# Kernel optimization log

Measured on AMD Instinct MI355X. Metric: run time of the kernel, lower is better.

The kernel has to match this reference:

```python
import jax, jax.numpy as jnp
import numpy as np

DIM = 2048
HEAD_DIM = 128
H = DIM // HEAD_DIM          # num ttt heads = 16
D_H = 128                    # inter_multi = 1.0 -> d_h = head_dim
CHUNK = 2048                 # lact_chunk_size
B, L = 1, 8192
BASE_LR = 0.01
LN_EPS = 1e-6                # flax LayerNorm default
NS_COEFS = [(4.0848, -6.8946, 2.927), (3.9505, -6.3029, 2.6377),
            (3.7418, -5.5913, 2.3037), (2.8769, -3.1427, 1.2046),
            (2.8366, -3.0525, 1.2012)]


def silu(x):
    return x * jax.nn.sigmoid(x)


def silu_backprop(dy, x):
    s = jax.nn.sigmoid(x)
    return dy * s * (1 + x * (1 - s))


def l2_norm(x, eps=1e-5):
    return x / (jnp.linalg.norm(x, axis=-1, keepdims=True) + eps)


def zeropower_ns5(G):
    # 5-step Newton-Schulz orthogonalization on a batch of matrices (bh, m, n)
    X = G
    transposed = G.shape[1] > G.shape[2]
    if transposed:
        X = jnp.swapaxes(X, 1, 2)
    X = X / (jnp.linalg.norm(X, axis=(1, 2), keepdims=True) + 1e-7)
    for a, b, c in NS_COEFS:
        A = X @ jnp.swapaxes(X, 1, 2)
        Bm = b * A + c * (A @ A)
        X = a * X + Bm @ X
    if transposed:
        X = jnp.swapaxes(X, 1, 2)
    return X


def block_causal_lact_swiglu(w0, w1, w2, q, k, v, lr0, lr1, lr2, momentum):
    # w0,w2: (bh, d_h, d); w1: (bh, d, d_h); q,k,v: (bh, l, d); lr*: (bh, l, 1)
    bh, l, d = k.shape
    v = jnp.swapaxes(v, 1, 2)   # (bh, d, l)
    q = jnp.swapaxes(q, 1, 2)   # (bh, d, l)
    w0_norm = jnp.linalg.norm(w0, axis=2, keepdims=True)
    w1_norm = jnp.linalg.norm(w1, axis=2, keepdims=True)
    w2_norm = jnp.linalg.norm(w2, axis=2, keepdims=True)
    outs = []
    for i in range(0, l - CHUNK, CHUNK):
        s, e = i, i + CHUNK
        ki = k[:, s:e, :]                      # (bh, C, d)
        vi = v[:, :, s:e]                      # (bh, d, C)
        qi = q[:, :, s:e]                      # (bh, d, C)
        lr0i, lr1i, lr2i = lr0[:, s:e, :], lr1[:, s:e, :], lr2[:, s:e, :]
        # apply current fast weights to queries
        h = w2 @ qi                            # (bh, d_h, C)
        gate = silu(w0 @ qi)
        outs.append(w1 @ (gate * h))           # (bh, d, C)
        # manual SwiGLU backprop through keys to get fast-weight grads
        kiT = jnp.swapaxes(ki, 1, 2)           # (bh, d, C)
        gate_before = w0 @ kiT                 # (bh, d_h, C)
        hidden_before = w2 @ kiT               # (bh, d_h, C)
        hidden = silu(gate_before) * hidden_before
        dhidden = jnp.swapaxes(w1, 1, 2) @ vi  # (bh, d_h, C)
        dhidden_before = dhidden * silu(gate_before)
        dgate = dhidden * hidden_before
        dgate_before = silu_backprop(dgate, gate_before)
        lr1iT = jnp.swapaxes(lr1i, 1, 2)       # (bh, 1, C) per-token lr
        dw1 = vi @ jnp.swapaxes(hidden * lr1iT, 1, 2)   # (bh, d, d_h)
        dw0 = dgate_before @ (ki * lr0i)                # (bh, d_h, d)
        dw2 = dhidden_before @ (ki * lr2i)              # (bh, d_h, d)
        if momentum is not None:
            m_i = jnp.mean(momentum[:, s:e, :], axis=1, keepdims=True)  # (bh,1,1)
            dw0 = dw0 + dw0 * m_i
            dw1 = dw1 + dw1 * m_i
            dw2 = dw2 + dw2 * m_i
        dw0 = zeropower_ns5(dw0)
        dw1 = zeropower_ns5(dw1)
        dw2 = zeropower_ns5(dw2)
        w0 = w0 + dw0
        w1 = w1 + dw1
        w2 = w2 + dw2
        # renormalize rows back to the initial norms
        w0 = w0 / (jnp.linalg.norm(w0, axis=2, keepdims=True) + 1e-5) * w0_norm
        w1 = w1 / (jnp.linalg.norm(w1, axis=2, keepdims=True) + 1e-5) * w1_norm
        w2 = w2 / (jnp.linalg.norm(w2, axis=2, keepdims=True) + 1e-5) * w2_norm
    # final chunk: apply only
    qi = q[:, :, l - CHUNK:]
    h = w2 @ qi
    gate = silu(w0 @ qi)
    outs.append(w1 @ (gate * h))
    out = jnp.concatenate(outs, axis=2)        # (bh, d, l)
    return jnp.swapaxes(out, 1, 2)             # (bh, l, d)


def _forward(x, W_qkv, W_lr, W_o, W_m, b_m, W_s, b_s, ln_g, ln_b, w0, w1, w2):
    b, l, _ = x.shape
    h, d = H, HEAD_DIM
    qkv = silu(x @ W_qkv).reshape(b, l, h, 3 * d)
    ttt_q, ttt_k, ttt_v = jnp.split(qkv, 3, axis=-1)
    ttt_q = l2_norm(ttt_q).reshape(b * h, l, d)
    ttt_k = l2_norm(ttt_k).reshape(b * h, l, d)
    ttt_v = ttt_v.reshape(b * h, l, d)
    base_lr_inv = BASE_LR + jnp.log(-jnp.expm1(jnp.float32(-BASE_LR)))
    lr = jax.nn.softplus(x @ W_lr + base_lr_inv)                 # (b, l, 3h)
    lr = lr.reshape(b, l, 3, h).transpose(2, 0, 3, 1).reshape(3, b * h, l, 1)
    lr0, lr1, lr2 = lr[0], lr[1], lr[2]
    w0b = jnp.tile(w0, (b, 1, 1))
    w1b = jnp.tile(w1, (b, 1, 1))
    w2b = jnp.tile(w2, (b, 1, 1))
    momentum = jax.nn.sigmoid(x @ W_m + b_m)                     # (b, l, h)
    momentum = momentum.reshape(b, l, h, 1).transpose(0, 2, 1, 3).reshape(b * h, l, 1)
    out = block_causal_lact_swiglu(w0b, w1b, w2b, ttt_q, ttt_k, ttt_v,
                                   lr0, lr1, lr2, momentum)      # (bh, l, d)
    # LayerNorm over last dim (flax default eps)
    mu = jnp.mean(out, axis=-1, keepdims=True)
    var = jnp.mean(jnp.square(out - mu), axis=-1, keepdims=True)
    out = (out - mu) * jax.lax.rsqrt(var + LN_EPS) * ln_g + ln_b
    scale = silu(x @ W_s + b_s).reshape(b, l, h, 1).transpose(0, 2, 1, 3).reshape(b * h, l, 1)
    out = out * scale
    out = out.reshape(b, h, l, d).transpose(0, 2, 1, 3).reshape(b, l, h * d)
    return out @ W_o


def setup_inputs() -> dict:
    ks = jax.random.split(jax.random.key(0), 11)
    sd = 1.0 / np.sqrt(DIM)
    return {
        "x": jax.random.normal(ks[0], (B, L, DIM), jnp.float32),
        "W_qkv": jax.random.normal(ks[1], (DIM, 3 * DIM), jnp.float32) * sd,
        "W_lr": jax.random.normal(ks[2], (DIM, 3 * H), jnp.float32) * sd,
        "W_o": jax.random.normal(ks[3], (DIM, DIM), jnp.float32) * sd,
        "W_m": jax.random.normal(ks[4], (DIM, H), jnp.float32) * sd,
        "b_m": jnp.zeros((H,), jnp.float32),
        "W_s": jax.random.normal(ks[5], (DIM, H), jnp.float32) * sd,
        "b_s": jnp.zeros((H,), jnp.float32),
        "ln_g": jnp.ones((HEAD_DIM,), jnp.float32),
        "ln_b": jnp.zeros((HEAD_DIM,), jnp.float32),
        "w0": jax.random.normal(ks[6], (H, D_H, HEAD_DIM), jnp.float32) / np.sqrt(HEAD_DIM),
        "w1": jax.random.normal(ks[7], (H, HEAD_DIM, D_H), jnp.float32) / np.sqrt(D_H),
        "w2": jax.random.normal(ks[8], (H, D_H, HEAD_DIM), jnp.float32) / np.sqrt(HEAD_DIM),
    }


def reference(x, W_qkv, W_lr, W_o, W_m, b_m, W_s, b_s, ln_g, ln_b, w0, w1, w2):
    return _forward(x, W_qkv, W_lr, W_o, W_m, b_m, W_s, b_s, ln_g, ln_b, w0, w1, w2)
```

## Files before the change

kernel.cpp:

```cpp
#include <hip/hip_runtime.h>
#include <hip/hip_bf16.h>
#include <cstdint>
#include <cstddef>

#define LSEQ   8192
#define DMODEL 2048
#define NH     16
#define HD     128
#define CH     2048

typedef __attribute__((ext_vector_type(8))) __bf16 bf16x8;
typedef __attribute__((ext_vector_type(4))) float f32x4;


__device__ __forceinline__ float wave_sum64(float v) {
#pragma unroll
  for (int m = 32; m; m >>= 1) v += __shfl_xor(v, m, 64);
  return v;
}

__device__ __forceinline__ float sigm(float x) { return 1.0f / (1.0f + expf(-x)); }

__device__ __forceinline__ unsigned short f2bf(float f) {
  unsigned int u = __float_as_uint(f);
  u += 0x7FFFu + ((u >> 16) & 1u);
  return (unsigned short)(u >> 16);
}
__device__ __forceinline__ float bf2f(unsigned short h) {
  return __uint_as_float((unsigned int)h << 16);
}

__device__ __forceinline__ void gload_lds16(const void* g, void* l) {
  __builtin_amdgcn_global_load_lds((__attribute__((address_space(1))) void*)(g),
                                   (__attribute__((address_space(3))) void*)(l), 16, 0, 0);
}

union bfu8 { bf16x8 v; unsigned short u[8]; };


__global__ void k_cast(const float* __restrict__ X, unsigned short* __restrict__ Xb, int n4) {
  int i = blockIdx.x * 256 + threadIdx.x;
  int stride = gridDim.x * 256;
  for (; i < n4; i += stride) {
    float4 v = ((const float4*)X)[i];
    ushort4 o;
    o.x = f2bf(v.x); o.y = f2bf(v.y); o.z = f2bf(v.z); o.w = f2bf(v.w);
    ((ushort4*)Xb)[i] = o;
  }
}

__global__ void k_tcast(const float* __restrict__ W, unsigned short* __restrict__ Wt,
                        int K, int N) {
  __shared__ float t[64][65];
  const int n0 = blockIdx.x * 64, k0 = blockIdx.y * 64;
  const int tid = threadIdx.x;
  const int cx = tid & 63, ry = tid >> 6;
#pragma unroll
  for (int r = 0; r < 16; ++r) {
    int row = ry + r * 4;
    t[row][cx] = W[(size_t)(k0 + row) * N + n0 + cx];
  }
  __syncthreads();
#pragma unroll
  for (int r = 0; r < 16; ++r) {
    int nn = ry + r * 4;
    Wt[(size_t)(n0 + nn) * K + k0 + cx] = f2bf(t[cx][nn]);
  }
}


__device__ __forceinline__ void gemm_core(const unsigned short* __restrict__ A,
                                          const unsigned short* __restrict__ B,
                                          int K, int ldA, int ldB, int row0, int col0,
                                          unsigned short* Al, unsigned short* Bl,
                                          f32x4 acc[4][4]) {
  const int tid = threadIdx.x;
  const int w = tid >> 6, l = tid & 63;
  const int lrow = l & 15, lk = (l >> 4) * 8;
  const int wr = (w >> 1) * 64, wc = (w & 1) * 64;
  const int srow = l >> 2, skk = (l & 3) * 8;

  for (int kk = 0; kk < K; kk += 32) {
#pragma unroll
    for (int q = 0; q < 2; ++q) {
      int c = w * 2 + q;
      gload_lds16(A + (size_t)(row0 + c * 16 + srow) * ldA + kk + skk, &Al[c * 512]);
      gload_lds16(B + (size_t)(col0 + c * 16 + srow) * ldB + kk + skk, &Bl[c * 512]);
    }
    __syncthreads();
    bf16x8 af[4], bfr[4];
#pragma unroll
    for (int m = 0; m < 4; ++m)
      af[m] = *(const bf16x8*)&Al[(wr + m * 16 + lrow) * 32 + lk];
#pragma unroll
    for (int n = 0; n < 4; ++n)
      bfr[n] = *(const bf16x8*)&Bl[(wc + n * 16 + lrow) * 32 + lk];
#pragma unroll
    for (int m = 0; m < 4; ++m)
#pragma unroll
      for (int n = 0; n < 4; ++n)
        acc[m][n] = __builtin_amdgcn_mfma_f32_16x16x32_bf16(af[m], bfr[n], acc[m][n], 0, 0, 0);
    __syncthreads();
  }
}


__device__ __forceinline__ bf16x8 ld_sw(const unsigned short* base, int row, int kcol) {
  int byte = (row * 256 + kcol * 2) ^ ((row & 7) << 4);
  return *(const bf16x8*)((const char*)base + byte);
}
__device__ __forceinline__ void st_sw(unsigned short* base, int row, int col, unsigned short v) {
  int byte = (row * 256 + col * 2) ^ ((row & 7) << 4);
  *(unsigned short*)((char*)base + byte) = v;
}
__device__ __forceinline__ unsigned short ld_sw1(const unsigned short* base, int row, int col) {
  int byte = (row * 256 + col * 2) ^ ((row & 7) << 4);
  return *(const unsigned short*)((const char*)base + byte);
}

__device__ __forceinline__ void stage_sw(const float* __restrict__ src, int ld,
                                         unsigned short* dst, int tid) {
#pragma unroll
  for (int p = 0; p < 16; ++p) {
    int row = p * 8 + (tid >> 5);
    int col = (tid & 31) * 4;
    float4 v = *(const float4*)(src + (size_t)row * ld + col);
    int byte = (row * 256 + col * 2) ^ ((row & 7) << 4);
    unsigned short* d = (unsigned short*)((char*)dst + byte);
    d[0] = f2bf(v.x); d[1] = f2bf(v.y); d[2] = f2bf(v.z); d[3] = f2bf(v.w);
  }
}

__device__ __forceinline__ void stage_hl(const float* __restrict__ src, int ld,
                                         unsigned short* H, unsigned short* L, int tid) {
#pragma unroll
  for (int p = 0; p < 16; ++p) {
    int row = p * 8 + (tid >> 5);
    int col = (tid & 31) * 4;
    float4 v = *(const float4*)(src + (size_t)row * ld + col);
    int byte = (row * 256 + col * 2) ^ ((row & 7) << 4);
    unsigned short* h = (unsigned short*)((char*)H + byte);
    unsigned short* l = (unsigned short*)((char*)L + byte);
    const float* pv = (const float*)&v;
#pragma unroll
    for (int i = 0; i < 4; ++i) {
      unsigned short hi = f2bf(pv[i]);
      h[i] = hi;
      l[i] = f2bf(pv[i] - bf2f(hi));
    }
  }
}

__device__ __forceinline__ void stage_hl_1024(const float* __restrict__ src, int ld,
                                              unsigned short* H, unsigned short* L, int tid) {
#pragma unroll
  for (int p = 0; p < 4; ++p) {
    int row = p * 32 + (tid >> 5);
    int col = (tid & 31) * 4;
    float4 v = *(const float4*)(src + (size_t)row * ld + col);
    int byte = (row * 256 + col * 2) ^ ((row & 7) << 4);
    unsigned short* h = (unsigned short*)((char*)H + byte);
    unsigned short* l = (unsigned short*)((char*)L + byte);
    const float* pv = (const float*)&v;
#pragma unroll
    for (int i = 0; i < 4; ++i) {
      unsigned short hi = f2bf(pv[i]);
      h[i] = hi;
      l[i] = f2bf(pv[i] - bf2f(hi));
    }
  }
}

__device__ __forceinline__ void stage_hl_ts(const float* __restrict__ src, int ld,
                                            const float* __restrict__ lr,
                                            unsigned short* H, unsigned short* L, int tid) {
#pragma unroll
  for (int p = 0; p < 16; ++p) {
    int t = p * 8 + (tid >> 5);
    int d = (tid & 31) * 4;
    float4 v = *(const float4*)(src + (size_t)t * ld + d);
    float sc = lr[t];
    const float* pv = (const float*)&v;
#pragma unroll
    for (int i = 0; i < 4; ++i) {
      float x = pv[i] * sc;
      unsigned short hi = f2bf(x);
      st_sw(H, d + i, t, hi);
      st_sw(L, d + i, t, f2bf(x - bf2f(hi)));
    }
  }
}


__global__ void k_init_w(const float* __restrict__ w0, const float* __restrict__ w1,
                         const float* __restrict__ w2, float* __restrict__ WW,
                         float* __restrict__ WN0, float* __restrict__ W1T) {
  int rid = blockIdx.x;
  int m = rid >> 11;
  int gr = rid & 2047;
  const float* src = (m == 0) ? w0 : (m == 1) ? w1 : w2;
  const float* row = src + (size_t)gr * HD;
  float* drow = WW + ((size_t)m * 2048 + gr) * HD;
  int l = threadIdx.x;
  float v0 = row[l], v1 = row[l + 64];
  drow[l] = v0; drow[l + 64] = v1;
  if (m == 1) {
    int g = gr >> 7, r = gr & 127;
    W1T[((size_t)g * 128 + l) * 128 + r] = v0;
    W1T[((size_t)g * 128 + l + 64) * 128 + r] = v1;
  }
  float s = wave_sum64(v0 * v0 + v1 * v1);
  if (l == 0) WN0[rid] = sqrtf(s);
}


__global__ __launch_bounds__(256) void k_qkv_mfma(const unsigned short* __restrict__ xb,
                                                  const unsigned short* __restrict__ Wqt,
                                                  float* __restrict__ Q, float* __restrict__ Km,
                                                  float* __restrict__ V) {
  __shared__ unsigned short Al[128 * 32];
  __shared__ unsigned short Bl[128 * 32];
  f32x4 acc[4][4];
#pragma unroll
  for (int m = 0; m < 4; ++m)
#pragma unroll
    for (int n = 0; n < 4; ++n) acc[m][n] = {};

  gemm_core(xb, Wqt, DMODEL, DMODEL, DMODEL, blockIdx.x * 128, blockIdx.y * 128, Al, Bl, acc);

  const int ct = blockIdx.y, hh = ct / 3, which = ct % 3;
  float* dst = (which == 0) ? Q : (which == 1) ? Km : V;
  const int tid = threadIdx.x, w = tid >> 6, l = tid & 63;
  const int wr = (w >> 1) * 64, wc = (w & 1) * 64;
#pragma unroll
  for (int m = 0; m < 4; ++m)
#pragma unroll
    for (int j = 0; j < 4; ++j) {
      int t = blockIdx.x * 128 + wr + m * 16 + (l >> 4) * 4 + j;
      int fth = t * NH + hh;
      int g = fth >> 13, tp = fth & 8191;
      float* drow = dst + ((size_t)g * LSEQ + tp) * HD;
#pragma unroll
      for (int n = 0; n < 4; ++n) {
        float v = acc[m][n][j];
        drow[wc + n * 16 + (l & 15)] = v * sigm(v);
      }
    }
}

__global__ void k_l2norm(float* __restrict__ Q, float* __restrict__ Km) {
  int rid = blockIdx.x * 4 + (threadIdx.x >> 6);
  int l = threadIdx.x & 63;
  float* base = (rid < NH * LSEQ) ? Q : Km;
  int r = (rid < NH * LSEQ) ? rid : rid - NH * LSEQ;
  float* row = base + (size_t)r * HD;
  float v0 = row[l], v1 = row[l + 64];
  float s = wave_sum64(v0 * v0 + v1 * v1);
  float f = 1.0f / (sqrtf(s) + 1e-5f);
  row[l] = v0 * f;
  row[l + 64] = v1 * f;
}


__global__ __launch_bounds__(256) void k_lrms5(const float* __restrict__ x,
                                               const float* __restrict__ Wlr,
                                               const float* __restrict__ Wsc,
                                               float* __restrict__ P) {
  __shared__ float Xs[128][67];
  __shared__ float Ws[128][68];
  const int tb = blockIdx.x;
  const int kp = blockIdx.y;
  const int tid = threadIdx.x;
  for (int i = tid; i < 128 * 64; i += 256) {
    int k = i >> 6, c = i & 63;
    float wv = (c < 48) ? Wlr[(size_t)(kp * 128 + k) * 48 + c]
                        : Wsc[(size_t)(kp * 128 + k) * 16 + (c - 48)];
    Ws[k][c] = wv;
  }
  const int t8 = tid >> 5, kk = tid & 31;
#pragma unroll
  for (int r = 0; r < 8; ++r) {
    int t = t8 + r * 8;
    float4 v = *(const float4*)(x + (size_t)(tb * 64 + t) * DMODEL + kp * 128 + kk * 4);
    Xs[kk * 4 + 0][t] = v.x; Xs[kk * 4 + 1][t] = v.y;
    Xs[kk * 4 + 2][t] = v.z; Xs[kk * 4 + 3][t] = v.w;
  }
  __syncthreads();
  const int ty = tid >> 4, tx = tid & 15;
  float acc[4][4];
#pragma unroll
  for (int i = 0; i < 4; ++i)
#pragma unroll
    for (int j = 0; j < 4; ++j) acc[i][j] = 0.0f;
  for (int k = 0; k < 128; ++k) {
    float a[4], b[4];
#pragma unroll
    for (int i = 0; i < 4; ++i) a[i] = Xs[k][ty * 4 + i];
#pragma unroll
    for (int j = 0; j < 4; ++j) b[j] = Ws[k][tx * 4 + j];
#pragma unroll
    for (int i = 0; i < 4; ++i)
#pragma unroll
      for (int j = 0; j < 4; ++j) acc[i][j] = fmaf(a[i], b[j], acc[i][j]);
  }
  float* o = P + ((size_t)tb * 16 + kp) * 4096;
#pragma unroll
  for (int i = 0; i < 4; ++i)
#pragma unroll
    for (int j = 0; j < 4; ++j)
      o[(ty * 4 + i) * 64 + tx * 4 + j] = acc[i][j];
}

__global__ void k_lrsum(const float* __restrict__ P, const float* __restrict__ bs,
                        float* __restrict__ LR, float* __restrict__ SCL) {
  int e = blockIdx.x * 256 + threadIdx.x;
  int t = e >> 6, c = e & 63;
  const float* base = P + ((size_t)(t >> 6) * 16) * 4096 + (t & 63) * 64 + c;
  float sum = 0.0f;
#pragma unroll
  for (int kp = 0; kp < 16; ++kp) sum += base[(size_t)kp * 4096];
  if (c < 48) {
    float base_lr_inv = 0.01f + logf(-expm1f(-0.01f));
    float v = sum + base_lr_inv;
    float sp = fmaxf(v, 0.0f) + log1pf(expf(-fabsf(v)));
    LR[(size_t)c * LSEQ + t] = sp;
  } else {
    float v = sum + bs[c - 48];
    SCL[(size_t)(c - 48) * LSEQ + t] = v * sigm(v);
  }
}


__global__ __launch_bounds__(256) void k_out2(const float* __restrict__ WW,
                                              const float* __restrict__ Q,
                                              const float* __restrict__ SCL,
                                              const float* __restrict__ lng,
                                              const float* __restrict__ lnb,
                                              unsigned short* __restrict__ U, int s) {
  __shared__ __align__(16) char smem[131072];
  unsigned short* Qs  = (unsigned short*)smem;
  unsigned short* W0s = (unsigned short*)(smem + 32768);
  unsigned short* W2s = (unsigned short*)(smem + 65536);
  unsigned short* GHs = (unsigned short*)(smem + 98304);
  float* Os = (float*)smem;

  const int g = blockIdx.y;
  const int t0 = blockIdx.x * 128;
  const int tid = threadIdx.x;
  const int w = tid >> 6, l = tid & 63;
  const int lrow = l & 15, lk8 = (l >> 4) * 8;
  const int wr = (w >> 1) * 64, wc = (w & 1) * 64;

  const float* Qg  = Q + ((size_t)g * LSEQ + s + t0) * HD;
  const float* w0g = WW + ((size_t)0 * 2048 + g * 128) * 128;
  const float* w1g = WW + ((size_t)1 * 2048 + g * 128) * 128;
  const float* w2g = WW + ((size_t)2 * 2048 + g * 128) * 128;

  stage_sw(Qg, HD, Qs, tid);
  stage_sw(w0g, 128, W0s, tid);
  stage_sw(w2g, 128, W2s, tid);
  __syncthreads();

  f32x4 ga[4][4], ha[4][4];
#pragma unroll
  for (int m = 0; m < 4; ++m)
#pragma unroll
    for (int n = 0; n < 4; ++n) { ga[m][n] = {}; ha[m][n] = {}; }
#pragma unroll
  for (int kk = 0; kk < 128; kk += 32) {
    bf16x8 af[4], b0[4], b2[4];
#pragma unroll
    for (int m = 0; m < 4; ++m) af[m] = ld_sw(Qs, wr + m * 16 + lrow, kk + lk8);
#pragma unroll
    for (int n = 0; n < 4; ++n) {
      b0[n] = ld_sw(W0s, wc + n * 16 + lrow, kk + lk8);
      b2[n] = ld_sw(W2s, wc + n * 16 + lrow, kk + lk8);
    }
#pragma unroll
    for (int m = 0; m < 4; ++m)
#pragma unroll
      for (int n = 0; n < 4; ++n) {
        ga[m][n] = __builtin_amdgcn_mfma_f32_16x16x32_bf16(af[m], b0[n], ga[m][n], 0, 0, 0);
        ha[m][n] = __builtin_amdgcn_mfma_f32_16x16x32_bf16(af[m], b2[n], ha[m][n], 0, 0, 0);
      }
  }
#pragma unroll
  for (int m = 0; m < 4; ++m)
#pragma unroll
    for (int n = 0; n < 4; ++n)
#pragma unroll
      for (int j = 0; j < 4; ++j) {
        int row = wr + m * 16 + (l >> 4) * 4 + j;
        int col = wc + n * 16 + (l & 15);
        float gv = ga[m][n][j];
        st_sw(GHs, row, col, f2bf(gv * sigm(gv) * ha[m][n][j]));
      }
  __syncthreads();
  stage_sw(w1g, 128, W0s, tid);
  __syncthreads();

  f32x4 oa[4][4];
#pragma unroll
  for (int m = 0; m < 4; ++m)
#pragma unroll
    for (int n = 0; n < 4; ++n) oa[m][n] = {};
#pragma unroll
  for (int kk = 0; kk < 128; kk += 32) {
    bf16x8 af[4], b1[4];
#pragma unroll
    for (int m = 0; m < 4; ++m) af[m] = ld_sw(GHs, wr + m * 16 + lrow, kk + lk8);
#pragma unroll
    for (int n = 0; n < 4; ++n) b1[n] = ld_sw(W0s, wc + n * 16 + lrow, kk + lk8);
#pragma unroll
    for (int m = 0; m < 4; ++m)
#pragma unroll
      for (int n = 0; n < 4; ++n)
        oa[m][n] = __builtin_amdgcn_mfma_f32_16x16x32_bf16(af[m], b1[n], oa[m][n], 0, 0, 0);
  }
  __syncthreads();
#pragma unroll
  for (int m = 0; m < 4; ++m)
#pragma unroll
    for (int n = 0; n < 4; ++n)
#pragma unroll
      for (int j = 0; j < 4; ++j) {
        int row = wr + m * 16 + (l >> 4) * 4 + j;
        int col = wc + n * 16 + (l & 15);
        Os[row * 132 + col] = oa[m][n][j];
      }
  __syncthreads();

  const int tok = tid >> 1, part = tid & 1;
  const float* orow = Os + tok * 132 + part * 64;
  float sum = 0.0f;
#pragma unroll
  for (int q = 0; q < 16; ++q) {
    float4 v = *(const float4*)(orow + q * 4);
    sum += (v.x + v.y) + (v.z + v.w);
  }
  sum += __shfl_xor(sum, 1, 64);
  float mu = sum * (1.0f / 128.0f);
  float vs = 0.0f;
#pragma unroll
  for (int q = 0; q < 16; ++q) {
    float4 v = *(const float4*)(orow + q * 4);
    float d0 = v.x - mu, d1 = v.y - mu, d2 = v.z - mu, d3 = v.w - mu;
    vs += d0 * d0 + d1 * d1 + d2 * d2 + d3 * d3;
  }
  vs += __shfl_xor(vs, 1, 64);
  float rstd = rsqrtf(vs * (1.0f / 128.0f) + 1e-6f);
  int tabs = s + t0 + tok;
  float sc = SCL[(size_t)g * LSEQ + tabs];
  unsigned short* urow = U + (size_t)tabs * DMODEL + g * HD + part * 64;
#pragma unroll
  for (int q = 0; q < 16; ++q) {
    float4 v = *(const float4*)(orow + q * 4);
    int d = part * 64 + q * 4;
    ushort4 o;
    o.x = f2bf(((v.x - mu) * rstd * lng[d + 0] + lnb[d + 0]) * sc);
    o.y = f2bf(((v.y - mu) * rstd * lng[d + 1] + lnb[d + 1]) * sc);
    o.z = f2bf(((v.z - mu) * rstd * lng[d + 2] + lnb[d + 2]) * sc);
    o.w = f2bf(((v.w - mu) * rstd * lng[d + 3] + lnb[d + 3]) * sc);
    *(ushort4*)(urow + q * 4) = o;
  }
}

__global__ __launch_bounds__(1024) void k_fe(const float* __restrict__ WW,
                                             const float* __restrict__ W1T,
                                             const float* __restrict__ Km,
                                             const float* __restrict__ V,
                                             float* __restrict__ BUF, int s) {
  __shared__ __align__(16) char smem[131072];
  unsigned short* KH = (unsigned short*)smem;
  unsigned short* KL = (unsigned short*)(smem + 32768);
  unsigned short* VH = (unsigned short*)(smem + 65536);
  unsigned short* VL = (unsigned short*)(smem + 98304);

  const int tt0 = blockIdx.x * 128;
  const int g = blockIdx.y;
  const int tid = threadIdx.x;
  const int w = tid >> 6, l = tid & 63;
  const int ww = w >> 2, wv = w & 3;
  const int lrow = l & 15, lk8 = (l >> 4) * 8;
  const int frow = (l >> 4) * 4, fcol = l & 15;

  stage_hl_1024(Km + ((size_t)g * LSEQ + s + tt0) * HD, HD, KH, KL, tid);
  stage_hl_1024(V + ((size_t)g * LSEQ + s + tt0) * HD, HD, VH, VL, tid);
  __syncthreads();

  const float* Asrc[3];
  Asrc[0] = WW + ((size_t)0 * 2048 + g * 128) * 128;
  Asrc[1] = WW + ((size_t)2 * 2048 + g * 128) * 128;
  Asrc[2] = W1T + (size_t)g * 16384;

  f32x4 acc[3][2][2];
#pragma unroll
  for (int q = 0; q < 3; ++q)
#pragma unroll
    for (int m = 0; m < 2; ++m)
#pragma unroll
      for (int n = 0; n < 2; ++n) acc[q][m][n] = {};

#pragma unroll 1
  for (int q = 0; q < 3; ++q) {
    const float* src = Asrc[q];
    const unsigned short* BH = (q == 2) ? VH : KH;
    const unsigned short* BL = (q == 2) ? VL : KL;
#pragma unroll
    for (int kk = 0; kk < 128; kk += 32) {
      bf16x8 ah[2], al[2], bh[2], bl[2];
#pragma unroll
      for (int m = 0; m < 2; ++m) {
        int row = ww * 32 + m * 16 + lrow;
        float4 v0 = *(const float4*)(src + (size_t)row * 128 + kk + lk8);
        float4 v1 = *(const float4*)(src + (size_t)row * 128 + kk + lk8 + 4);
        bfu8 h, lo;
        const float* p0 = (const float*)&v0;
        const float* p1 = (const float*)&v1;
#pragma unroll
        for (int i = 0; i < 4; ++i) {
          unsigned short hb0 = f2bf(p0[i]);
          h.u[i] = hb0; lo.u[i] = f2bf(p0[i] - bf2f(hb0));
          unsigned short hb1 = f2bf(p1[i]);
          h.u[i + 4] = hb1; lo.u[i + 4] = f2bf(p1[i] - bf2f(hb1));
        }
        ah[m] = h.v; al[m] = lo.v;
      }
#pragma unroll
      for (int n = 0; n < 2; ++n) {
        int row = wv * 32 + n * 16 + lrow;
        bh[n] = ld_sw(BH, row, kk + lk8);
        bl[n] = ld_sw(BL, row, kk + lk8);
      }
#pragma unroll
      for (int m = 0; m < 2; ++m)
#pragma unroll
        for (int n = 0; n < 2; ++n) {
          acc[q][m][n] = __builtin_amdgcn_mfma_f32_16x16x32_bf16(ah[m], bh[n], acc[q][m][n], 0, 0, 0);
          acc[q][m][n] = __builtin_amdgcn_mfma_f32_16x16x32_bf16(ah[m], bl[n], acc[q][m][n], 0, 0, 0);
          acc[q][m][n] = __builtin_amdgcn_mfma_f32_16x16x32_bf16(al[m], bh[n], acc[q][m][n], 0, 0, 0);
        }
    }
  }

  float* out0 = BUF + (size_t)0 * (NH * 128 * CH) + (size_t)g * 128 * CH;
  float* out1 = BUF + (size_t)1 * (NH * 128 * CH) + (size_t)g * 128 * CH;
  float* out2 = BUF + (size_t)2 * (NH * 128 * CH) + (size_t)g * 128 * CH;
#pragma unroll
  for (int m = 0; m < 2; ++m)
#pragma unroll
    for (int n = 0; n < 2; ++n)
#pragma unroll
      for (int j = 0; j < 4; ++j) {
        int row = ww * 32 + m * 16 + frow + j;
        int col = wv * 32 + n * 16 + fcol;
        float gb = acc[0][m][n][j];
        float hb = acc[1][m][n][j];
        float dh = acc[2][m][n][j];
        float sg = sigm(gb);
        float sgb = gb * sg;
        float hid = sgb * hb;
        float dgate = dh * hb;
        float dgb = dgate * sg * (1.0f + gb * (1.0f - sg));
        float dhb = dh * sgb;
        size_t o = (size_t)row * CH + tt0 + col;
        out0[o] = hid; out1[o] = dgb; out2[o] = dhb;
      }
}

__global__ __launch_bounds__(256) void k_dwp_mx(const float* __restrict__ BUF,
                                                const float* __restrict__ Km,
                                                const float* __restrict__ V,
                                                const float* __restrict__ LR,
                                                float* __restrict__ DWP, int s) {
  __shared__ __align__(16) char smem[131072];
  unsigned short* AH = (unsigned short*)smem;
  unsigned short* AL = (unsigned short*)(smem + 32768);
  unsigned short* BH = (unsigned short*)(smem + 65536);
  unsigned short* BL = (unsigned short*)(smem + 98304);

  const int p = blockIdx.x;
  const int g = blockIdx.y;
  const int z = blockIdx.z;
  const int tid = threadIdx.x;
  const int w = tid >> 6, l = tid & 63;
  const int lrow = l & 15, lk8 = (l >> 4) * 8;
  const int wr = (w >> 1) * 64, wc = (w & 1) * 64;

  const int msel = (z == 0) ? 1 : (z == 1) ? 0 : 2;
  const float* M = BUF + (size_t)msel * (NH * 128 * CH) + (size_t)g * 128 * CH;
  const float* N = (z == 1) ? V : Km;
  const float* lr = LR + (size_t)(z * NH + g) * LSEQ;
  const int ts = p * 256;

  f32x4 acc[4][4];
#pragma unroll
  for (int m = 0; m < 4; ++m)
#pragma unroll
    for (int n = 0; n < 4; ++n) acc[m][n] = {};

  for (int h = 0; h < 2; ++h) {
    if (h) __syncthreads();
    stage_hl(M + ts + h * 128, CH, AH, AL, tid);
    stage_hl_ts(N + ((size_t)g * LSEQ + s + ts + h * 128) * HD, HD,
                lr + s + ts + h * 128, BH, BL, tid);
    __syncthreads();
#pragma unroll
    for (int kk = 0; kk < 128; kk += 32) {
      bf16x8 ah[4], al4[4], bh[4], bl4[4];
#pragma unroll
      for (int m = 0; m < 4; ++m) {
        ah[m] = ld_sw(AH, wr + m * 16 + lrow, kk + lk8);
        al4[m] = ld_sw(AL, wr + m * 16 + lrow, kk + lk8);
      }
#pragma unroll
      for (int n = 0; n < 4; ++n) {
        bh[n] = ld_sw(BH, wc + n * 16 + lrow, kk + lk8);
        bl4[n] = ld_sw(BL, wc + n * 16 + lrow, kk + lk8);
      }
#pragma unroll
      for (int m = 0; m < 4; ++m)
#pragma unroll
        for (int n = 0; n < 4; ++n) {
          acc[m][n] = __builtin_amdgcn_mfma_f32_16x16x32_bf16(ah[m], bh[n], acc[m][n], 0, 0, 0);
          acc[m][n] = __builtin_amdgcn_mfma_f32_16x16x32_bf16(ah[m], bl4[n], acc[m][n], 0, 0, 0);
          acc[m][n] = __builtin_amdgcn_mfma_f32_16x16x32_bf16(al4[m], bh[n], acc[m][n], 0, 0, 0);
        }
    }
  }

  float* outp = DWP + (((size_t)(z * NH + g)) * 8 + p) * 16384;
#pragma unroll
  for (int m = 0; m < 4; ++m)
#pragma unroll
    for (int n = 0; n < 4; ++n)
#pragma unroll
      for (int j = 0; j < 4; ++j) {
        int row = wr + m * 16 + (l >> 4) * 4 + j;
        int col = wc + n * 16 + (l & 15);
        outp[row * 128 + col] = acc[m][n][j];
      }
}

__global__ void k_dwred(const float* __restrict__ DWP, float* __restrict__ DW) {
  int zg = blockIdx.x;
  int z = zg >> 4;
  const float* base = DWP + (size_t)zg * 8 * 16384;
  float* out = DW + (size_t)zg * 16384;
  for (int idx = threadIdx.x; idx < 16384; idx += 256) {
    float sv = 0.0f;
#pragma unroll
    for (int pp = 0; pp < 8; ++pp) sv += base[(size_t)pp * 16384 + idx];
    int oidx = (z == 1) ? ((idx & 127) * 128 + (idx >> 7)) : idx;
    out[oidx] = sv;
  }
}

__global__ __launch_bounds__(1024) void k_ns5_mfma(float* __restrict__ DW) {
  __shared__ __align__(16) char smem[131072];
  unsigned short* PH = (unsigned short*)smem;
  unsigned short* PL = (unsigned short*)(smem + 32768);
  unsigned short* QH = (unsigned short*)(smem + 65536);
  unsigned short* QL = (unsigned short*)(smem + 98304);
  float* red = (float*)(smem + 65536);

  const float NA[5] = {4.0848f, 3.9505f, 3.7418f, 2.8769f, 2.8366f};
  const float NB[5] = {-6.8946f, -6.3029f, -5.5913f, -3.1427f, -3.0525f};
  const float NC[5] = {2.927f, 2.6377f, 2.3037f, 1.2046f, 1.2012f};
  float* Gm = DW + (size_t)blockIdx.x * 16384;
  const int tid = threadIdx.x;
  const int w = tid >> 6, l = tid & 63;
  const int ww = w >> 2, wv = w & 3;
  const int lrow = l & 15, lk8 = (l >> 4) * 8;
  const int frow = (l >> 4) * 4, fcol = l & 15;

  float vals[16];
  float psum = 0.0f;
#pragma unroll
  for (int r = 0; r < 16; ++r) {
    vals[r] = Gm[tid + r * 1024];
    psum = fmaf(vals[r], vals[r], psum);
  }
  psum = wave_sum64(psum);
  if (l == 0) red[w] = psum;
  __syncthreads();
  float tot = 0.0f;
#pragma unroll
  for (int i = 0; i < 16; ++i) tot += red[i];
  float scl = 1.0f / (sqrtf(tot) + 1e-7f);
  __syncthreads();
#pragma unroll
  for (int r = 0; r < 16; ++r) {
    int idx = tid + r * 1024;
    int rr = idx >> 7, cc = idx & 127;
    float v = vals[r] * scl;
    unsigned short hi = f2bf(v);
    st_sw(PH, rr, cc, hi);
    st_sw(PL, rr, cc, f2bf(v - bf2f(hi)));
  }
  __syncthreads();

#pragma unroll 1
  for (int it = 0; it < 5; ++it) {
    const float ac = NA[it], bc = NB[it], cc2 = NC[it];

    f32x4 accA[2][2];
#pragma unroll
    for (int m = 0; m < 2; ++m)
#pragma unroll
      for (int n = 0; n < 2; ++n) accA[m][n] = {};
#pragma unroll
    for (int kk = 0; kk < 128; kk += 32) {
      bf16x8 ah[2], al[2], bh[2], bl[2];
#pragma unroll
      for (int m = 0; m < 2; ++m) {
        ah[m] = ld_sw(PH, ww * 32 + m * 16 + lrow, kk + lk8);
        al[m] = ld_sw(PL, ww * 32 + m * 16 + lrow, kk + lk8);
      }
#pragma unroll
      for (int n = 0; n < 2; ++n) {
        bh[n] = ld_sw(PH, wv * 32 + n * 16 + lrow, kk + lk8);
        bl[n] = ld_sw(PL, wv * 32 + n * 16 + lrow, kk + lk8);
      }
#pragma unroll
      for (int m = 0; m < 2; ++m)
#pragma unroll
        for (int n = 0; n < 2; ++n) {
          accA[m][n] = __builtin_amdgcn_mfma_f32_16x16x32_bf16(ah[m], bh[n], accA[m][n], 0, 0, 0);
          accA[m][n] = __builtin_amdgcn_mfma_f32_16x16x32_bf16(ah[m], bl[n], accA[m][n], 0, 0, 0);
          accA[m][n] = __builtin_amdgcn_mfma_f32_16x16x32_bf16(al[m], bh[n], accA[m][n], 0, 0, 0);
        }
    }
#pragma unroll
    for (int m = 0; m < 2; ++m)
#pragma unroll
      for (int n = 0; n < 2; ++n)
#pragma unroll
        for (int j = 0; j < 4; ++j) {
          int row = ww * 32 + m * 16 + frow + j;
          int col = wv * 32 + n * 16 + fcol;
          float v = accA[m][n][j];
          unsigned short hi = f2bf(v);
          st_sw(QH, row, col, hi);
          st_sw(QL, row, col, f2bf(v - bf2f(hi)));
        }
    __syncthreads();

    f32x4 accB[2][2];
#pragma unroll
    for (int m = 0; m < 2; ++m)
#pragma unroll
      for (int n = 0; n < 2; ++n) accB[m][n] = {};
#pragma unroll
    for (int kk = 0; kk < 128; kk += 32) {
      bf16x8 ah[2], al[2], bh[2], bl[2];
#pragma unroll
      for (int m = 0; m < 2; ++m) {
        ah[m] = ld_sw(QH, ww * 32 + m * 16 + lrow, kk + lk8);
        al[m] = ld_sw(QL, ww * 32 + m * 16 + lrow, kk + lk8);
      }
#pragma unroll
      for (int n = 0; n < 2; ++n) {
        bh[n] = ld_sw(QH, wv * 32 + n * 16 + lrow, kk + lk8);
        bl[n] = ld_sw(QL, wv * 32 + n * 16 + lrow, kk + lk8);
      }
#pragma unroll
      for (int m = 0; m < 2; ++m)
#pragma unroll
        for (int n = 0; n < 2; ++n) {
          accB[m][n] = __builtin_amdgcn_mfma_f32_16x16x32_bf16(ah[m], bh[n], accB[m][n], 0, 0, 0);
          accB[m][n] = __builtin_amdgcn_mfma_f32_16x16x32_bf16(ah[m], bl[n], accB[m][n], 0, 0, 0);
          accB[m][n] = __builtin_amdgcn_mfma_f32_16x16x32_bf16(al[m], bh[n], accB[m][n], 0, 0, 0);
        }
    }
#pragma unroll
    for (int m = 0; m < 2; ++m)
#pragma unroll
      for (int n = 0; n < 2; ++n)
#pragma unroll
        for (int j = 0; j < 4; ++j)
          accB[m][n][j] = fmaf(bc, accA[m][n][j], cc2 * accB[m][n][j]);
    __syncthreads();
#pragma unroll
    for (int m = 0; m < 2; ++m)
#pragma unroll
      for (int n = 0; n < 2; ++n)
#pragma unroll
        for (int j = 0; j < 4; ++j) {
          int row = ww * 32 + m * 16 + frow + j;
          int col = wv * 32 + n * 16 + fcol;
          float v = accB[m][n][j];
          unsigned short hi = f2bf(v);
          st_sw(QH, row, col, hi);
          st_sw(QL, row, col, f2bf(v - bf2f(hi)));
        }
    unsigned short th[16], tl[16];
#pragma unroll
    for (int r = 0; r < 16; ++r) {
      int idx = tid + r * 1024;
      int rr = idx >> 7, ccx = idx & 127;
      th[r] = ld_sw1(PH, rr, ccx);
      tl[r] = ld_sw1(PL, rr, ccx);
    }
    __syncthreads();
#pragma unroll
    for (int r = 0; r < 16; ++r) {
      int idx = tid + r * 1024;
      int rr = idx >> 7, ccx = idx & 127;
      st_sw(PH, ccx, rr, th[r]);
      st_sw(PL, ccx, rr, tl[r]);
    }
    __syncthreads();

    f32x4 accC[2][2];
#pragma unroll
    for (int m = 0; m < 2; ++m)
#pragma unroll
      for (int n = 0; n < 2; ++n) accC[m][n] = {};
#pragma unroll
    for (int kk = 0; kk < 128; kk += 32) {
      bf16x8 ah[2], al[2], bh[2], bl[2];
#pragma unroll
      for (int m = 0; m < 2; ++m) {
        ah[m] = ld_sw(PH, ww * 32 + m * 16 + lrow, kk + lk8);
        al[m] = ld_sw(PL, ww * 32 + m * 16 + lrow, kk + lk8);
      }
#pragma unroll
      for (int n = 0; n < 2; ++n) {
        bh[n] = ld_sw(QH, wv * 32 + n * 16 + lrow, kk + lk8);
        bl[n] = ld_sw(QL, wv * 32 + n * 16 + lrow, kk + lk8);
      }
#pragma unroll
      for (int m = 0; m < 2; ++m)
#pragma unroll
        for (int n = 0; n < 2; ++n) {
          accC[m][n] = __builtin_amdgcn_mfma_f32_16x16x32_bf16(ah[m], bh[n], accC[m][n], 0, 0, 0);
          accC[m][n] = __builtin_amdgcn_mfma_f32_16x16x32_bf16(ah[m], bl[n], accC[m][n], 0, 0, 0);
          accC[m][n] = __builtin_amdgcn_mfma_f32_16x16x32_bf16(al[m], bh[n], accC[m][n], 0, 0, 0);
        }
    }
#pragma unroll
    for (int m = 0; m < 2; ++m)
#pragma unroll
      for (int n = 0; n < 2; ++n)
#pragma unroll
        for (int j = 0; j < 4; ++j) {
          int row = ww * 32 + m * 16 + frow + j;
          int col = wv * 32 + n * 16 + fcol;
          float yv = bf2f(ld_sw1(PH, row, col)) + bf2f(ld_sw1(PL, row, col));
          accC[m][n][j] = fmaf(ac, yv, accC[m][n][j]);
        }
    __syncthreads();
#pragma unroll
    for (int m = 0; m < 2; ++m)
#pragma unroll
      for (int n = 0; n < 2; ++n)
#pragma unroll
        for (int j = 0; j < 4; ++j) {
          int row = ww * 32 + m * 16 + frow + j;
          int col = wv * 32 + n * 16 + fcol;
          float v = accC[m][n][j];
          unsigned short hi = f2bf(v);
          st_sw(PH, row, col, hi);
          st_sw(PL, row, col, f2bf(v - bf2f(hi)));
        }
    __syncthreads();
  }

#pragma unroll
  for (int r = 0; r < 16; ++r) {
    int idx = tid + r * 1024;
    int rr = idx >> 7, ccx = idx & 127;
    Gm[idx] = bf2f(ld_sw1(PH, ccx, rr)) + bf2f(ld_sw1(PL, ccx, rr));
  }
}

__global__ void k_apply(float* __restrict__ WW, const float* __restrict__ DW,
                        const float* __restrict__ WN0, float* __restrict__ W1T) {
  int rid = blockIdx.x;
  int m = rid >> 11;
  int gr = rid & 2047;
  int l = threadIdx.x;
  float* wrow = WW + (size_t)rid * 128;
  const float* drow = DW + (size_t)rid * 128;
  float v0 = wrow[l] + drow[l];
  float v1 = wrow[l + 64] + drow[l + 64];
  float s = wave_sum64(v0 * v0 + v1 * v1);
  float f = WN0[rid] / (sqrtf(s) + 1e-5f);
  v0 *= f; v1 *= f;
  wrow[l] = v0;
  wrow[l + 64] = v1;
  if (m == 1) {
    int g = gr >> 7, r = gr & 127;
    W1T[((size_t)g * 128 + l) * 128 + r] = v0;
    W1T[((size_t)g * 128 + l + 64) * 128 + r] = v1;
  }
}


__global__ __launch_bounds__(256) void k_final_mfma(const unsigned short* __restrict__ U,
                                                    const unsigned short* __restrict__ Wot,
                                                    float* __restrict__ out) {
  __shared__ unsigned short Al[128 * 32];
  __shared__ unsigned short Bl[128 * 32];
  f32x4 acc[4][4];
#pragma unroll
  for (int m = 0; m < 4; ++m)
#pragma unroll
    for (int n = 0; n < 4; ++n) acc[m][n] = {};

  const int row0 = blockIdx.x * 128, col0 = blockIdx.y * 128;
  gemm_core(U, Wot, DMODEL, DMODEL, DMODEL, row0, col0, Al, Bl, acc);

  const int tid = threadIdx.x, w = tid >> 6, l = tid & 63;
  const int wr = (w >> 1) * 64, wc = (w & 1) * 64;
#pragma unroll
  for (int m = 0; m < 4; ++m)
#pragma unroll
    for (int j = 0; j < 4; ++j) {
      int t = row0 + wr + m * 16 + (l >> 4) * 4 + j;
      float* orow = out + (size_t)t * DMODEL + col0;
#pragma unroll
      for (int n = 0; n < 4; ++n)
        orow[wc + n * 16 + (l & 15)] = acc[m][n][j];
    }
}


extern "C" void kernel_launch(void* const* d_in, const int* in_sizes, int n_in,
                              void* d_out, int out_size, void* d_ws, size_t ws_size,
                              hipStream_t stream) {
  (void)in_sizes; (void)n_in; (void)out_size;
  const float* x    = (const float*)d_in[0];
  const float* Wqkv = (const float*)d_in[1];
  const float* Wlr  = (const float*)d_in[2];
  const float* Wo   = (const float*)d_in[3];
  const float* Wsc  = (const float*)d_in[6];
  const float* bs   = (const float*)d_in[7];
  const float* lng  = (const float*)d_in[8];
  const float* lnb  = (const float*)d_in[9];
  const float* w0   = (const float*)d_in[10];
  const float* w1   = (const float*)d_in[11];
  const float* w2   = (const float*)d_in[12];

  float* Q = (float*)d_out;

  float* ws = (float*)d_ws;
  size_t off = 0;
  auto alloc = [&](size_t n) { float* p = ws + off; off += n; return p; };
  float* Km   = alloc((size_t)NH * LSEQ * HD);
  float* V    = alloc((size_t)NH * LSEQ * HD);
  float* Uf   = alloc((size_t)LSEQ * DMODEL / 2);
  float* LR   = alloc((size_t)3 * NH * LSEQ);
  float* SCL  = alloc((size_t)NH * LSEQ);
  float* WW   = alloc((size_t)3 * NH * HD * HD);
  float* WN0  = alloc((size_t)3 * NH * HD);
  float* W1T  = alloc((size_t)NH * HD * HD);
  float* BUF  = alloc((size_t)3 * NH * HD * CH);
  float* DW   = alloc((size_t)3 * NH * HD * HD);
  float* DWP  = alloc((size_t)3 * NH * 8 * HD * HD);
  if (off * sizeof(float) > ws_size) return;

  unsigned short* U = (unsigned short*)Uf;
  unsigned short* xb  = (unsigned short*)BUF;
  unsigned short* Wqt = (unsigned short*)(BUF + (size_t)LSEQ * DMODEL / 2);
  float* Plr = BUF;
  unsigned short* Wot = (unsigned short*)BUF;

  k_init_w<<<3 * NH * HD, 64, 0, stream>>>(w0, w1, w2, WW, WN0, W1T);
  k_cast<<<2048, 256, 0, stream>>>(x, xb, LSEQ * DMODEL / 4);
  k_tcast<<<dim3(3 * DMODEL / 64, DMODEL / 64), 256, 0, stream>>>(Wqkv, Wqt, DMODEL, 3 * DMODEL);
  k_qkv_mfma<<<dim3(LSEQ / 128, 48), 256, 0, stream>>>(xb, Wqt, Q, Km, V);
  k_l2norm<<<2 * NH * LSEQ / 4, 256, 0, stream>>>(Q, Km);
  k_lrms5<<<dim3(LSEQ / 64, 16), 256, 0, stream>>>(x, Wlr, Wsc, Plr);
  k_lrsum<<<LSEQ * 64 / 256, 256, 0, stream>>>(Plr, bs, LR, SCL);

  for (int c = 0; c < 4; ++c) {
    int s = c * CH;
    k_out2<<<dim3(CH / 128, NH), 256, 0, stream>>>(WW, Q, SCL, lng, lnb, U, s);
    if (c < 3) {
      k_fe<<<dim3(CH / 128, NH), 1024, 0, stream>>>(WW, W1T, Km, V, BUF, s);
      k_dwp_mx<<<dim3(8, NH, 3), 256, 0, stream>>>(BUF, Km, V, LR, DWP, s);
      k_dwred<<<3 * NH, 256, 0, stream>>>(DWP, DW);
      k_ns5_mfma<<<3 * NH, 1024, 0, stream>>>(DW);
      k_apply<<<3 * NH * HD, 64, 0, stream>>>(WW, DW, WN0, W1T);
    }
  }
  k_tcast<<<dim3(DMODEL / 64, DMODEL / 64), 256, 0, stream>>>(Wo, Wot, DMODEL, DMODEL);
  k_final_mfma<<<dim3(LSEQ / 128, DMODEL / 128), 256, 0, stream>>>(U, Wot, (float*)d_out);
}
```

Before: 1.402 ms.

## Fuse L2 norm into QKV GEMM epilogue, merge DW reduction into NS5, swizzle grids

The QKV GEMM epilogue now computes per-row squared norms across the two column waves through shared memory and writes L2-normalised Q and K directly, which removes the separate l2norm pass over Q and K. The partial-gradient reduction (and the transpose for w1) is folded into the Newton-Schulz kernel's load and store, dropping one kernel launch and one DW round trip per chunk. Both big GEMMs switch to a flat 1D grid with a block-index swizzle meant to improve L2 reuse. These add a __syncthreads and extra shuffles to the GEMM epilogue and repeated strided partial reads inside the NS5 kernel.

New measurement: 1.375 ms. Within noise of the previous version (-1.9%).

```diff
diff --git a/kernel.cpp b/kernel.cpp
--- a/kernel.cpp
+++ b/kernel.cpp
@@ -220,45 +220,83 @@
                                                   float* __restrict__ V) {
   __shared__ unsigned short Al[128 * 32];
   __shared__ unsigned short Bl[128 * 32];
+  __shared__ float nrm[128][2];
+  const int flat = blockIdx.x;
+  const int swz = (flat & 7) * 384 + (flat >> 3);
+  const int bx = swz & 63, ct = swz >> 6;
+
   f32x4 acc[4][4];
 #pragma unroll
   for (int m = 0; m < 4; ++m)
 #pragma unroll
     for (int n = 0; n < 4; ++n) acc[m][n] = {};
 
-  gemm_core(xb, Wqt, DMODEL, DMODEL, DMODEL, blockIdx.x * 128, blockIdx.y * 128, Al, Bl, acc);
-
-  const int ct = blockIdx.y, hh = ct / 3, which = ct % 3;
+  gemm_core(xb, Wqt, DMODEL, DMODEL, DMODEL, bx * 128, ct * 128, Al, Bl, acc);
+
+  const int hh = ct / 3, which = ct % 3;
   float* dst = (which == 0) ? Q : (which == 1) ? Km : V;
   const int tid = threadIdx.x, w = tid >> 6, l = tid & 63;
   const int wr = (w >> 1) * 64, wc = (w & 1) * 64;
+
 #pragma unroll
   for (int m = 0; m < 4; ++m)
 #pragma unroll
+    for (int n = 0; n < 4; ++n)
+#pragma unroll
+      for (int j = 0; j < 4; ++j) {
+        float v = acc[m][n][j];
+        acc[m][n][j] = v * sigm(v);
+      }
+
+  float f[4][4];
+  if (which != 2) {
+#pragma unroll
+    for (int m = 0; m < 4; ++m)
+#pragma unroll
+      for (int j = 0; j < 4; ++j) {
+        float p = 0.0f;
+#pragma unroll
+        for (int n = 0; n < 4; ++n) p = fmaf(acc[m][n][j], acc[m][n][j], p);
+        p += __shfl_xor(p, 1, 64);
+        p += __shfl_xor(p, 2, 64);
+        p += __shfl_xor(p, 4, 64);
+        p += __shfl_xor(p, 8, 64);
+        f[m][j] = p;
+      }
+    if ((l & 15) == 0) {
+#pragma unroll
+      for (int m = 0; m < 4; ++m)
+#pragma unroll
+        for (int j = 0; j < 4; ++j)
+          nrm[wr + m * 16 + (l >> 4) * 4 + j][w & 1] = f[m][j];
+    }
+    __syncthreads();
+#pragma unroll
+    for (int m = 0; m < 4; ++m)
+#pragma unroll
+      for (int j = 0; j < 4; ++j) {
+        int row = wr + m * 16 + (l >> 4) * 4 + j;
+        f[m][j] = 1.0f / (sqrtf(nrm[row][0] + nrm[row][1]) + 1e-5f);
+      }
+  } else {
+#pragma unroll
+    for (int m = 0; m < 4; ++m)
+#pragma unroll
+      for (int j = 0; j < 4; ++j) f[m][j] = 1.0f;
+  }
+
+#pragma unroll
+  for (int m = 0; m < 4; ++m)
+#pragma unroll
     for (int j = 0; j < 4; ++j) {
-      int t = blockIdx.x * 128 + wr + m * 16 + (l >> 4) * 4 + j;
+      int t = bx * 128 + wr + m * 16 + (l >> 4) * 4 + j;
       int fth = t * NH + hh;
       int g = fth >> 13, tp = fth & 8191;
       float* drow = dst + ((size_t)g * LSEQ + tp) * HD;
 #pragma unroll
-      for (int n = 0; n < 4; ++n) {
-        float v = acc[m][n][j];
-        drow[wc + n * 16 + (l & 15)] = v * sigm(v);
-      }
-    }
-}
-
-__global__ void k_l2norm(float* __restrict__ Q, float* __restrict__ Km) {
-  int rid = blockIdx.x * 4 + (threadIdx.x >> 6);
-  int l = threadIdx.x & 63;
-  float* base = (rid < NH * LSEQ) ? Q : Km;
-  int r = (rid < NH * LSEQ) ? rid : rid - NH * LSEQ;
-  float* row = base + (size_t)r * HD;
-  float v0 = row[l], v1 = row[l + 64];
-  float s = wave_sum64(v0 * v0 + v1 * v1);
-  float f = 1.0f / (sqrtf(s) + 1e-5f);
-  row[l] = v0 * f;
-  row[l + 64] = v1 * f;
+      for (int n = 0; n < 4; ++n)
+        drow[wc + n * 16 + (l & 15)] = acc[m][n][j] * f[m][j];
+    }
 }
 
 
@@ -465,6 +503,7 @@
   }
 }
 
+
 __global__ __launch_bounds__(1024) void k_fe(const float* __restrict__ WW,
                                              const float* __restrict__ W1T,
                                              const float* __restrict__ Km,
@@ -642,21 +681,8 @@
       }
 }
 
-__global__ void k_dwred(const float* __restrict__ DWP, float* __restrict__ DW) {
-  int zg = blockIdx.x;
-  int z = zg >> 4;
-  const float* base = DWP + (size_t)zg * 8 * 16384;
-  float* out = DW + (size_t)zg * 16384;
-  for (int idx = threadIdx.x; idx < 16384; idx += 256) {
-    float sv = 0.0f;
-#pragma unroll
-    for (int pp = 0; pp < 8; ++pp) sv += base[(size_t)pp * 16384 + idx];
-    int oidx = (z == 1) ? ((idx & 127) * 128 + (idx >> 7)) : idx;
-    out[oidx] = sv;
-  }
-}
-
-__global__ __launch_bounds__(1024) void k_ns5_mfma(float* __restrict__ DW) {
+__global__ __launch_bounds__(1024) void k_ns5_mfma(const float* __restrict__ DWP,
+                                                   float* __restrict__ DW) {
   __shared__ __align__(16) char smem[131072];
   unsigned short* PH = (unsigned short*)smem;
   unsigned short* PL = (unsigned short*)(smem + 32768);
@@ -667,7 +693,10 @@
   const float NA[5] = {4.0848f, 3.9505f, 3.7418f, 2.8769f, 2.8366f};
   const float NB[5] = {-6.8946f, -6.3029f, -5.5913f, -3.1427f, -3.0525f};
   const float NC[5] = {2.927f, 2.6377f, 2.3037f, 1.2046f, 1.2012f};
-  float* Gm = DW + (size_t)blockIdx.x * 16384;
+  const int zg = blockIdx.x;
+  const int z = zg >> 4;
+  const float* base = DWP + (size_t)zg * 8 * 16384;
+  float* Gout = DW + (size_t)zg * 16384;
   const int tid = threadIdx.x;
   const int w = tid >> 6, l = tid & 63;
   const int ww = w >> 2, wv = w & 3;
@@ -678,8 +707,12 @@
   float psum = 0.0f;
 #pragma unroll
   for (int r = 0; r < 16; ++r) {
-    vals[r] = Gm[tid + r * 1024];
-    psum = fmaf(vals[r], vals[r], psum);
+    int idx = tid + r * 1024;
+    float sv = 0.0f;
+#pragma unroll
+    for (int p = 0; p < 8; ++p) sv += base[(size_t)p * 16384 + idx];
+    vals[r] = sv;
+    psum = fmaf(sv, sv, psum);
   }
   psum = wave_sum64(psum);
   if (l == 0) red[w] = psum;
@@ -871,7 +904,10 @@
   for (int r = 0; r < 16; ++r) {
     int idx = tid + r * 1024;
     int rr = idx >> 7, ccx = idx & 127;
-    Gm[idx] = bf2f(ld_sw1(PH, ccx, rr)) + bf2f(ld_sw1(PL, ccx, rr));
+    if (z == 1)
+      Gout[idx] = bf2f(ld_sw1(PH, rr, ccx)) + bf2f(ld_sw1(PL, rr, ccx));
+    else
+      Gout[idx] = bf2f(ld_sw1(PH, ccx, rr)) + bf2f(ld_sw1(PL, ccx, rr));
   }
 }
 
@@ -909,7 +945,9 @@
 #pragma unroll
     for (int n = 0; n < 4; ++n) acc[m][n] = {};
 
-  const int row0 = blockIdx.x * 128, col0 = blockIdx.y * 128;
+  const int flat = blockIdx.x;
+  const int swz = (flat & 7) * 128 + (flat >> 3);
+  const int row0 = (swz & 63) * 128, col0 = (swz >> 6) * 128;
   gemm_core(U, Wot, DMODEL, DMODEL, DMODEL, row0, col0, Al, Bl, acc);
 
   const int tid = threadIdx.x, w = tid >> 6, l = tid & 63;
@@ -970,8 +1008,7 @@
   k_init_w<<<3 * NH * HD, 64, 0, stream>>>(w0, w1, w2, WW, WN0, W1T);
   k_cast<<<2048, 256, 0, stream>>>(x, xb, LSEQ * DMODEL / 4);
   k_tcast<<<dim3(3 * DMODEL / 64, DMODEL / 64), 256, 0, stream>>>(Wqkv, Wqt, DMODEL, 3 * DMODEL);
-  k_qkv_mfma<<<dim3(LSEQ / 128, 48), 256, 0, stream>>>(xb, Wqt, Q, Km, V);
-  k_l2norm<<<2 * NH * LSEQ / 4, 256, 0, stream>>>(Q, Km);
+  k_qkv_mfma<<<3072, 256, 0, stream>>>(xb, Wqt, Q, Km, V);
   k_lrms5<<<dim3(LSEQ / 64, 16), 256, 0, stream>>>(x, Wlr, Wsc, Plr);
   k_lrsum<<<LSEQ * 64 / 256, 256, 0, stream>>>(Plr, bs, LR, SCL);
 
@@ -981,11 +1018,10 @@
     if (c < 3) {
       k_fe<<<dim3(CH / 128, NH), 1024, 0, stream>>>(WW, W1T, Km, V, BUF, s);
       k_dwp_mx<<<dim3(8, NH, 3), 256, 0, stream>>>(BUF, Km, V, LR, DWP, s);
-      k_dwred<<<3 * NH, 256, 0, stream>>>(DWP, DW);
-      k_ns5_mfma<<<3 * NH, 1024, 0, stream>>>(DW);
+      k_ns5_mfma<<<3 * NH, 1024, 0, stream>>>(DWP, DW);
       k_apply<<<3 * NH * HD, 64, 0, stream>>>(WW, DW, WN0, W1T);
     }
   }
   k_tcast<<<dim3(DMODEL / 64, DMODEL / 64), 256, 0, stream>>>(Wo, Wot, DMODEL, DMODEL);
-  k_final_mfma<<<dim3(LSEQ / 128, DMODEL / 128), 256, 0, stream>>>(U, Wot, (float*)d_out);
-}
+  k_final_mfma<<<1024, 256, 0, stream>>>(U, Wot, (float*)d_out);
+}
```
